# Kernel optimization log

Hardware: AMD Instinct MI355X
Metric: run time of the kernel (lower is better)

The kernel has to match this reference:

```python
import jax, jax.numpy as jnp
import numpy as np

HIDDEN_DIM = 1024
NUM_HEADS = 16
HEAD_DIM = HIDDEN_DIM // NUM_HEADS
SCALAR_NORM = float(np.sqrt(HIDDEN_DIM / NUM_HEADS))


def setup_inputs() -> dict:
    key = jax.random.key(0)
    k1, k2 = jax.random.split(key)
    B, N, D = 2, 2048, HIDDEN_DIM
    x = jax.random.normal(k1, (B, N, D), dtype=jnp.float32)
    # torch Linear weight shape: (3D, D); xavier_uniform-like scale
    limit = float(np.sqrt(6.0 / (D + 3 * D)))
    W_qkv = jax.random.uniform(k2, (3 * D, D), dtype=jnp.float32, minval=-limit, maxval=limit)
    return {"x": x, "W_qkv": W_qkv}


def reference(x, W_qkv):
    b, n, d = x.shape
    h, hd = NUM_HEADS, HEAD_DIM
    qkv = x @ W_qkv.T  # (B, N, 3D)
    q, k, v = jnp.split(qkv, 3, axis=-1)
    # (B, H, N, hd)
    q = q.reshape(b, n, h, hd).transpose(0, 2, 1, 3)
    k = k.reshape(b, n, h, hd).transpose(0, 2, 1, 3)
    v = v.reshape(b, n, h, hd).transpose(0, 2, 1, 3)
    scores = jnp.einsum('bhik,bhjk->bhij', q, k) / SCALAR_NORM
    attn = jax.nn.softmax(scores, axis=-1)
    out = jnp.einsum('bhij,bhjk->bhik', attn, v)
    return out.transpose(0, 2, 1, 3).reshape(b, n, d)
```

## Files before the change

kernel.cpp:

```cpp
#include <hip/hip_runtime.h>
#include <hip/hip_bf16.h>

#define SEQ 2048
#define DMODEL 1024
#define NHEADS 16
#define HD 64
#define BATCH 2

typedef short bf16x8 __attribute__((ext_vector_type(8)));
typedef float f32x4 __attribute__((ext_vector_type(4)));
typedef float f32x16 __attribute__((ext_vector_type(16)));

static __device__ inline ushort f2bf(float f) {
    unsigned u = __float_as_uint(f);
    return (ushort)((u + 0x7fffu + ((u >> 16) & 1u)) >> 16);
}

static __device__ inline unsigned pk2bf(float a, float b) {
    __hip_bfloat162 h = __float22bfloat162_rn(make_float2(a, b));
    union { __hip_bfloat162 h; unsigned u; } c; c.h = h;
    return c.u;
}

static __device__ inline void async16(const ushort* g, ushort* l) {
    __builtin_amdgcn_global_load_lds((const __attribute__((address_space(1))) void*)g,
                                     (__attribute__((address_space(3))) void*)l, 16, 0, 0);
}

static __device__ inline void plane32swap(unsigned& a, unsigned& b) {
    asm volatile("v_permlane32_swap_b32 %0, %1" : "+v"(a), "+v"(b));
}

__global__ void cvt2(const float* __restrict__ a, ushort* __restrict__ da, int na,
                     const float* __restrict__ b, ushort* __restrict__ db, int nb) {
    long i = (long)(blockIdx.x * blockDim.x + threadIdx.x) * 4;
    const float* s; ushort* d;
    if (i < na) { s = a + i; d = da + i; }
    else { long j = i - na; if (j >= nb) return; s = b + j; d = db + j; }
    float4 v = *(const float4*)s;
    ushort4 o; o.x = f2bf(v.x); o.y = f2bf(v.y); o.z = f2bf(v.z); o.w = f2bf(v.w);
    *(ushort4*)d = o;
}

union GemmSmem {
    struct { ushort A[128 * 64]; ushort B[128 * 64]; } st;
    ushort C[128 * 128];
};

__global__ __launch_bounds__(256) void qkv_gemm(
        const ushort* __restrict__ X, const ushort* __restrict__ W,
        ushort* __restrict__ Qd, ushort* __restrict__ Kd, ushort* __restrict__ Vd) {
    __shared__ GemmSmem sm;
    const int t = threadIdx.x;
    const int lane = t & 63, l15 = lane & 15, quad = lane >> 4;
    const int w = t >> 6, wm = w >> 1, wn = w & 1;
    const int gm = blockIdx.x, gn = blockIdx.y;
    const int srow = t >> 3, scol = (t & 7) * 8;

    f32x4 acc[4][4] = {};

    for (int kt = 0; kt < 16; ++kt) {
        const int k0 = kt * 64;
        __syncthreads();
#pragma unroll
        for (int inst = 0; inst < 4; ++inst) {
            async16(&X[(gm * 128 + inst * 32 + srow) * 1024 + k0 + scol], &sm.st.A[inst * 2048 + t * 8]);
            async16(&W[(gn * 128 + inst * 32 + srow) * 1024 + k0 + scol], &sm.st.B[inst * 2048 + t * 8]);
        }
        __syncthreads();
#pragma unroll
        for (int ks = 0; ks < 2; ++ks) {
            const int kk = ks * 32 + quad * 8;
            bf16x8 af[4], bfr[4];
#pragma unroll
            for (int i = 0; i < 4; ++i) {
                af[i]  = *(const bf16x8*)&sm.st.A[(wm * 64 + i * 16 + l15) * 64 + kk];
                bfr[i] = *(const bf16x8*)&sm.st.B[(wn * 64 + i * 16 + l15) * 64 + kk];
            }
#pragma unroll
            for (int i = 0; i < 4; ++i)
#pragma unroll
                for (int j = 0; j < 4; ++j)
                    acc[i][j] = __builtin_amdgcn_mfma_f32_16x16x32_bf16(af[i], bfr[j], acc[i][j], 0, 0, 0);
        }
    }

    __syncthreads();
    const float sc = (gn < 8) ? (0.125f * 1.44269504f) : 1.0f;
#pragma unroll
    for (int i = 0; i < 4; ++i)
#pragma unroll
        for (int reg = 0; reg < 4; ++reg) {
            const int row = wm * 64 + i * 16 + quad * 4 + reg;
            const int sw = (row & 7) * 8;
#pragma unroll
            for (int jp = 0; jp < 4; jp += 2) {
                unsigned u = pk2bf(acc[i][jp][reg] * sc, acc[i][jp + 1][reg] * sc);
                sm.C[row * 128 + ((wn * 64 + jp * 16 + l15) ^ sw)] = (ushort)u;
                sm.C[row * 128 + ((wn * 64 + (jp + 1) * 16 + l15) ^ sw)] = (ushort)(u >> 16);
            }
        }
    __syncthreads();

    const int which = gn >> 3;
    ushort* dst = (which == 0) ? Qd : ((which == 1) ? Kd : Vd);
    const int rloc = t >> 4, l = t & 15;
#pragma unroll
    for (int pass = 0; pass < 8; ++pass) {
        const int r = pass * 16 + rloc;
        bf16x8 v = *(const bf16x8*)&sm.C[r * 128 + ((l * 8) ^ ((r & 7) * 8))];
        const int ng = gm * 128 + r;
        const int b = ng >> 11, n = ng & 2047;
        const int cl = (gn * 128 + l * 8) & 1023;
        const int h = cl >> 6, hd = cl & 63;
        *(bf16x8*)&dst[(((b * NHEADS + h) * SEQ) + n) * HD + hd] = v;
    }
}

__global__ __launch_bounds__(256) void tr_v(const ushort* __restrict__ src, ushort* __restrict__ dst) {
    __shared__ ushort sT[64][72];
    const int t = threadIdx.x;
    const int bh = blockIdx.y, nt = blockIdx.x;
    const int r0 = t >> 3, c8 = (t & 7) * 8;
    const ushort* sp = src + ((long)bh * SEQ + nt * 64) * HD;
#pragma unroll
    for (int rr = 0; rr < 64; rr += 32)
        *(bf16x8*)&sT[rr + r0][c8] = *(const bf16x8*)&sp[(rr + r0) * HD + c8];
    __syncthreads();
    ushort* dp = dst + (long)bh * HD * SEQ + nt * 64;
#pragma unroll
    for (int rr = 0; rr < 64; rr += 32) {
        const int hd = rr + r0;
        bf16x8 v;
#pragma unroll
        for (int j = 0; j < 8; ++j) v[j] = (short)sT[c8 + j][hd];
        *(bf16x8*)&dp[(long)hd * SEQ + c8] = v;
    }
}

__global__ __launch_bounds__(256, 2) void attn_kernel(
        const ushort* __restrict__ Q, const ushort* __restrict__ K,
        const ushort* __restrict__ VT, float* __restrict__ O) {
    __shared__ ushort sK[2][64 * 64];
    __shared__ ushort sVT[2][64 * 64];
    __shared__ float sL[4][32];

    const int t = threadIdx.x;
    const int lane = t & 63, l31 = lane & 31, hi = lane >> 5;
    const int w = t >> 6;

    const int flat = blockIdx.y * gridDim.x + blockIdx.x;
    const int qt = (flat >> 3) & 15;
    const int bh = (flat & 7) + ((flat >> 7) << 3);

    const ushort* Qp = Q + ((long)bh * SEQ + qt * 128 + w * 32) * HD;
    const ushort* Kp = K + (long)bh * SEQ * HD;
    const ushort* Vp = VT + (long)bh * HD * SEQ;

    bf16x8 bq[4];
#pragma unroll
    for (int ks = 0; ks < 4; ++ks)
        bq[ks] = *(const bf16x8*)&Qp[l31 * HD + ks * 16 + hi * 8];

    const int sr = t >> 3;
    const int scc = ((t & 7) ^ (sr & 7)) * 8;
    const ushort* gK = Kp + sr * HD + scc;
    const ushort* gV = Vp + (long)sr * SEQ + scc;
    ushort* lK[2] = { &sK[0][t * 8], &sK[1][t * 8] };
    ushort* lV[2] = { &sVT[0][t * 8], &sVT[1][t * 8] };

    f32x16 accO[2] = {};
    float Lp = 0.f;
    const int swz = (l31 & 7) << 3;

    async16(gK, lK[0]);
    async16(gK + 32 * HD, lK[0] + 32 * 64);
    async16(gV, lV[0]);
    async16(gV + 32 * SEQ, lV[0] + 32 * 64);
    __syncthreads();

    for (int kt = 0; kt < 32; ++kt) {
        const int cur = kt & 1;
        if (kt < 31) {
            const ushort* nK = gK + (kt + 1) * 64 * HD;
            const ushort* nV = gV + (kt + 1) * 64;
            async16(nK, lK[cur ^ 1]);
            async16(nK + 32 * HD, lK[cur ^ 1] + 32 * 64);
            async16(nV, lV[cur ^ 1]);
            async16(nV + 32 * SEQ, lV[cur ^ 1] + 32 * 64);
        }
        const ushort* bK = sK[cur];
        const ushort* bV = sVT[cur];

        f32x16 s[2];
#pragma unroll
        for (int nb = 0; nb < 2; ++nb) {
            f32x16 z = {};
            __builtin_amdgcn_s_setprio(1);
#pragma unroll
            for (int ks = 0; ks < 4; ++ks) {
                bf16x8 ak = *(const bf16x8*)&bK[(nb * 32 + l31) * 64 + ((ks * 16 + hi * 8) ^ swz)];
                z = __builtin_amdgcn_mfma_f32_32x32x16_bf16(ak, bq[ks], z, 0, 0, 0);
            }
            __builtin_amdgcn_s_setprio(0);
            s[nb] = z;
        }

        bf16x8 pa[4];
#pragma unroll
        for (int nb = 0; nb < 2; ++nb) {
            float p[16];
#pragma unroll
            for (int r = 0; r < 16; ++r) { p[r] = exp2f(s[nb][r]); Lp += p[r]; }
#pragma unroll
            for (int h2 = 0; h2 < 2; ++h2) {
                const int b = 8 * h2;
                unsigned c0 = pk2bf(p[b + 0], p[b + 1]);
                unsigned c1 = pk2bf(p[b + 2], p[b + 3]);
                unsigned c2 = pk2bf(p[b + 4], p[b + 5]);
                unsigned c3 = pk2bf(p[b + 6], p[b + 7]);
                plane32swap(c0, c2);
                plane32swap(c1, c3);
                union { unsigned u[4]; bf16x8 v; } f;
                f.u[0] = c0; f.u[1] = c1; f.u[2] = c2; f.u[3] = c3;
                pa[nb * 2 + h2] = f.v;
            }
        }

        __builtin_amdgcn_s_setprio(1);
#pragma unroll
        for (int db = 0; db < 2; ++db)
#pragma unroll
            for (int ks = 0; ks < 4; ++ks) {
                bf16x8 vf = *(const bf16x8*)&bV[(db * 32 + l31) * 64 + ((ks * 16 + hi * 8) ^ swz)];
                accO[db] = __builtin_amdgcn_mfma_f32_32x32x16_bf16(pa[ks], vf, accO[db], 0, 0, 0);
            }
        __builtin_amdgcn_s_setprio(0);

        __syncthreads();
    }

    unsigned lu = __float_as_uint(Lp), lv = lu;
    plane32swap(lu, lv);
    const float Ltot = __uint_as_float(lu) + __uint_as_float(lv);
    if (hi == 0) sL[w][l31] = Ltot;
    __syncthreads();

    const int b = bh >> 4, h = bh & 15;
    const int qg0 = qt * 128 + w * 32;
#pragma unroll
    for (int r = 0; r < 16; ++r) {
        const int ql = (r & 3) + 8 * (r >> 2) + 4 * hi;
        const float inv = 1.0f / sL[w][ql];
        const int row = qg0 + ql;
#pragma unroll
        for (int db = 0; db < 2; ++db)
            O[((long)b * SEQ + row) * DMODEL + h * HD + db * 32 + l31] = accO[db][r] * inv;
    }
}

extern "C" void kernel_launch(void* const* d_in, const int* in_sizes, int n_in,
                              void* d_out, int out_size, void* d_ws, size_t ws_size,
                              hipStream_t stream) {
    const float* x  = (const float*)d_in[0];
    const float* Wq = (const float*)d_in[1];
    float* out = (float*)d_out;

    const int NX = BATCH * SEQ * DMODEL;
    const int NW = 3 * DMODEL * DMODEL;
    const int NQKV = BATCH * NHEADS * SEQ * HD;

    ushort* xb = (ushort*)d_ws;
    ushort* wb = xb + NX;
    ushort* q  = wb + NW;
    ushort* k  = q + NQKV;
    ushort* vtmp = k + NQKV;
    ushort* vt = xb;

    cvt2<<<(NX + NW) / 4 / 256, 256, 0, stream>>>(x, xb, NX, Wq, wb, NW);

    dim3 g1(4096 / 128, 3072 / 128);
    qkv_gemm<<<g1, 256, 0, stream>>>(xb, wb, q, k, vtmp);

    dim3 gt(SEQ / 64, BATCH * NHEADS);
    tr_v<<<gt, 256, 0, stream>>>(vtmp, vt);

    dim3 g2(SEQ / 128, BATCH * NHEADS);
    attn_kernel<<<g2, 256, 0, stream>>>(q, k, vt, out);
}
```

Before: 178.4 us.

## Double KV tile to 128 keys per iteration, halving barriers and loop trips

```diff
diff --git a/kernel.cpp b/kernel.cpp
--- a/kernel.cpp
+++ b/kernel.cpp
@@ -141,8 +141,8 @@
 __global__ __launch_bounds__(256, 2) void attn_kernel(
         const ushort* __restrict__ Q, const ushort* __restrict__ K,
         const ushort* __restrict__ VT, float* __restrict__ O) {
-    __shared__ ushort sK[2][64 * 64];
-    __shared__ ushort sVT[2][64 * 64];
+    __shared__ ushort sK[2][128 * 64];
+    __shared__ ushort sVT[2][64 * 128];
     __shared__ float sL[4][32];
 
     const int t = threadIdx.x;
@@ -162,84 +162,94 @@
     for (int ks = 0; ks < 4; ++ks)
         bq[ks] = *(const bf16x8*)&Qp[l31 * HD + ks * 16 + hi * 8];
 
-    const int sr = t >> 3;
-    const int scc = ((t & 7) ^ (sr & 7)) * 8;
-    const ushort* gK = Kp + sr * HD + scc;
-    const ushort* gV = Vp + (long)sr * SEQ + scc;
+    const int krow = t >> 3;
+    const int kcol = ((t & 7) ^ (krow & 7)) * 8;
+    const ushort* gK = Kp + krow * HD + kcol;
+    const int vrow = t >> 4;
+    const int vcol = ((t & 15) ^ (vrow & 7)) * 8;
+    const ushort* gV = Vp + (long)vrow * SEQ + vcol;
+
     ushort* lK[2] = { &sK[0][t * 8], &sK[1][t * 8] };
     ushort* lV[2] = { &sVT[0][t * 8], &sVT[1][t * 8] };
 
     f32x16 accO[2] = {};
-    float Lp = 0.f;
+    f32x4 Lp4 = {};
     const int swz = (l31 & 7) << 3;
 
-    async16(gK, lK[0]);
-    async16(gK + 32 * HD, lK[0] + 32 * 64);
-    async16(gV, lV[0]);
-    async16(gV + 32 * SEQ, lV[0] + 32 * 64);
-    __syncthreads();
-
-    for (int kt = 0; kt < 32; ++kt) {
+#pragma unroll
+    for (int c = 0; c < 4; ++c) {
+        async16(gK + c * 32 * HD, lK[0] + c * 2048);
+        async16(gV + (long)c * 16 * SEQ, lV[0] + c * 2048);
+    }
+    __syncthreads();
+
+    for (int kt = 0; kt < 16; ++kt) {
         const int cur = kt & 1;
-        if (kt < 31) {
-            const ushort* nK = gK + (kt + 1) * 64 * HD;
-            const ushort* nV = gV + (kt + 1) * 64;
-            async16(nK, lK[cur ^ 1]);
-            async16(nK + 32 * HD, lK[cur ^ 1] + 32 * 64);
-            async16(nV, lV[cur ^ 1]);
-            async16(nV + 32 * SEQ, lV[cur ^ 1] + 32 * 64);
+        if (kt < 15) {
+            const ushort* nK = gK + (kt + 1) * 128 * HD;
+            const ushort* nV = gV + (kt + 1) * 128;
+#pragma unroll
+            for (int c = 0; c < 4; ++c) {
+                async16(nK + c * 32 * HD, lK[cur ^ 1] + c * 2048);
+                async16(nV + (long)c * 16 * SEQ, lV[cur ^ 1] + c * 2048);
+            }
         }
         const ushort* bK = sK[cur];
         const ushort* bV = sVT[cur];
 
-        f32x16 s[2];
-#pragma unroll
-        for (int nb = 0; nb < 2; ++nb) {
+        f32x16 s[4];
+        __builtin_amdgcn_s_setprio(1);
+#pragma unroll
+        for (int nb = 0; nb < 4; ++nb) {
             f32x16 z = {};
-            __builtin_amdgcn_s_setprio(1);
 #pragma unroll
             for (int ks = 0; ks < 4; ++ks) {
                 bf16x8 ak = *(const bf16x8*)&bK[(nb * 32 + l31) * 64 + ((ks * 16 + hi * 8) ^ swz)];
                 z = __builtin_amdgcn_mfma_f32_32x32x16_bf16(ak, bq[ks], z, 0, 0, 0);
             }
+            s[nb] = z;
+        }
+        __builtin_amdgcn_s_setprio(0);
+
+#pragma unroll
+        for (int h = 0; h < 2; ++h) {
+            bf16x8 pa[4];
+#pragma unroll
+            for (int nb = 0; nb < 2; ++nb) {
+                float p[16];
+#pragma unroll
+                for (int r = 0; r < 16; ++r) p[r] = exp2f(s[h * 2 + nb][r]);
+#pragma unroll
+                for (int r = 0; r < 16; ++r) Lp4[r & 3] += p[r];
+#pragma unroll
+                for (int h2 = 0; h2 < 2; ++h2) {
+                    const int b = 8 * h2;
+                    unsigned c0 = pk2bf(p[b + 0], p[b + 1]);
+                    unsigned c1 = pk2bf(p[b + 2], p[b + 3]);
+                    unsigned c2 = pk2bf(p[b + 4], p[b + 5]);
+                    unsigned c3 = pk2bf(p[b + 6], p[b + 7]);
+                    plane32swap(c0, c2);
+                    plane32swap(c1, c3);
+                    union { unsigned u[4]; bf16x8 v; } f;
+                    f.u[0] = c0; f.u[1] = c1; f.u[2] = c2; f.u[3] = c3;
+                    pa[nb * 2 + h2] = f.v;
+                }
+            }
+            __builtin_amdgcn_s_setprio(1);
+#pragma unroll
+            for (int db = 0; db < 2; ++db)
+#pragma unroll
+                for (int ks = 0; ks < 4; ++ks) {
+                    bf16x8 vf = *(const bf16x8*)&bV[(db * 32 + l31) * 128 + h * 64 + ((ks * 16 + hi * 8) ^ swz)];
+                    accO[db] = __builtin_amdgcn_mfma_f32_32x32x16_bf16(pa[ks], vf, accO[db], 0, 0, 0);
+                }
             __builtin_amdgcn_s_setprio(0);
-            s[nb] = z;
-        }
-
-        bf16x8 pa[4];
-#pragma unroll
-        for (int nb = 0; nb < 2; ++nb) {
-            float p[16];
-#pragma unroll
-            for (int r = 0; r < 16; ++r) { p[r] = exp2f(s[nb][r]); Lp += p[r]; }
-#pragma unroll
-            for (int h2 = 0; h2 < 2; ++h2) {
-                const int b = 8 * h2;
-                unsigned c0 = pk2bf(p[b + 0], p[b + 1]);
-                unsigned c1 = pk2bf(p[b + 2], p[b + 3]);
-                unsigned c2 = pk2bf(p[b + 4], p[b + 5]);
-                unsigned c3 = pk2bf(p[b + 6], p[b + 7]);
-                plane32swap(c0, c2);
-                plane32swap(c1, c3);
-                union { unsigned u[4]; bf16x8 v; } f;
-                f.u[0] = c0; f.u[1] = c1; f.u[2] = c2; f.u[3] = c3;
-                pa[nb * 2 + h2] = f.v;
-            }
-        }
-
-        __builtin_amdgcn_s_setprio(1);
-#pragma unroll
-        for (int db = 0; db < 2; ++db)
-#pragma unroll
-            for (int ks = 0; ks < 4; ++ks) {
-                bf16x8 vf = *(const bf16x8*)&bV[(db * 32 + l31) * 64 + ((ks * 16 + hi * 8) ^ swz)];
-                accO[db] = __builtin_amdgcn_mfma_f32_32x32x16_bf16(pa[ks], vf, accO[db], 0, 0, 0);
-            }
-        __builtin_amdgcn_s_setprio(0);
+        }
 
         __syncthreads();
     }
 
+    const float Lp = (Lp4[0] + Lp4[1]) + (Lp4[2] + Lp4[3]);
     unsigned lu = __float_as_uint(Lp), lv = lu;
     plane32swap(lu, lv);
     const float Ltot = __uint_as_float(lu) + __uint_as_float(lv);
```

New measurement: 177.7 us. No clear change (-0.4%).
